# Performance work log

Hardware: AMD Instinct MI355X
Metric: run time of the kernel (lower is better)

The kernel has to match this reference:

```python
import jax, jax.numpy as jnp
import numpy as np

VOXEL_SIZE = np.array([0.05, 0.05, 0.1], dtype=np.float32)
PCR = np.array([0.0, -40.0, -3.0, 70.4, 40.0, 1.0], dtype=np.float32)
MAX_POINTS = 32
MAX_VOXELS = 120000
N_POINTS = 2_000_000
NFEAT = 4

GRID = np.round((PCR[3:] - PCR[:3]) / VOXEL_SIZE).astype(np.int64)  # [gx, gy, gz] = [1408, 1600, 40]
GX, GY, GZ = int(GRID[0]), int(GRID[1]), int(GRID[2])
G_TOTAL = GX * GY * GZ  # sentinel linear id for invalid points


def setup_inputs() -> dict:
    key = jax.random.key(0)
    k1, k2 = jax.random.split(key)
    # xyz uniform inside the point-cloud range, reflectivity ~ U[0,1)
    xyz = jax.random.uniform(k1, (N_POINTS, 3), minval=jnp.asarray(PCR[:3]), maxval=jnp.asarray(PCR[3:]))
    feat = jax.random.uniform(k2, (N_POINTS, NFEAT - 3))
    points = jnp.concatenate([xyz, feat], axis=1).astype(jnp.float32)
    return {"points": points}


def reference(points):
    """Deterministic hard voxelization (mmcv hard_voxelize_forward).

    Returns padded fixed-shape outputs plus voxel_num (jit-compatible):
      voxels [MAX_VOXELS, MAX_POINTS, C], coors [MAX_VOXELS, 3] (z,y,x),
      num_points_per_voxel [MAX_VOXELS], voxel_num scalar.
    Rows >= voxel_num are zero padding (torch version slices them off).
    """
    N, C = points.shape
    vs = jnp.asarray(VOXEL_SIZE)
    lo = jnp.asarray(PCR[:3])

    # Voxel coordinate of each point (x, y, z order)
    c = jnp.floor((points[:, :3] - lo) / vs).astype(jnp.int32)  # [N,3]
    valid = jnp.all((c >= 0) & (c < jnp.array([GX, GY, GZ], jnp.int32)), axis=1)

    # Linear voxel id; invalid points -> sentinel G_TOTAL (sorts last)
    lin = (c[:, 2].astype(jnp.int64) * (GY * GX)
           + c[:, 1].astype(jnp.int64) * GX
           + c[:, 0].astype(jnp.int64))
    lin = jnp.where(valid, lin, G_TOTAL)

    # Stable sort by voxel id: within a voxel, points keep original order
    order = jnp.argsort(lin, stable=True)          # [N] original indices
    slin = lin[order]
    pos = jnp.arange(N)
    is_new = jnp.concatenate([jnp.array([True]), slin[1:] != slin[:-1]])  # group starts
    start_pos = jax.lax.cummax(jnp.where(is_new, pos, 0))  # start position of each point's group
    rank_in_group = pos - start_pos                         # arrival order within voxel
    valid_s = slin < G_TOTAL

    # Voxel slots are assigned in order of first point appearance (deterministic CUDA kernel).
    # At each group start, the group's first original point index is order[pos].
    group_key = jnp.where(is_new & valid_s, order, N)       # non-starts/invalid rank last
    slot_at_pos = jnp.argsort(jnp.argsort(group_key))       # rank among groups by first appearance
    slot = slot_at_pos[start_pos]                            # [N] voxel slot per point

    voxel_num = jnp.minimum(jnp.sum((is_new & valid_s).astype(jnp.int32)), MAX_VOXELS)

    keep = valid_s & (rank_in_group < MAX_POINTS) & (slot < MAX_VOXELS)
    slot_w = jnp.where(keep, slot, MAX_VOXELS)   # dropped points -> extra pad row
    rank_w = jnp.where(keep, rank_in_group, 0)

    voxels = jnp.zeros((MAX_VOXELS + 1, MAX_POINTS, C), points.dtype)
    voxels = voxels.at[slot_w, rank_w].set(points[order])[:MAX_VOXELS]

    czyx = c[order][:, ::-1]  # store coords in (z, y, x) order like mmcv
    coor_keep = is_new & valid_s & (slot < MAX_VOXELS)
    cslot = jnp.where(coor_keep, slot, MAX_VOXELS)
    coors = jnp.zeros((MAX_VOXELS + 1, 3), jnp.int32).at[cslot].set(czyx)[:MAX_VOXELS]

    num_points_per_voxel = (jnp.zeros((MAX_VOXELS + 1,), jnp.int32)
                            .at[slot_w].add(keep.astype(jnp.int32))[:MAX_VOXELS])

    return voxels, coors, num_points_per_voxel, voxel_num
```

## Files before the change

kernel.cpp:

```cpp
#include <hip/hip_runtime.h>


#define GX 1408
#define GY 1600
#define GZ 40
#define MAXV 120000
#define MAXP 32

#define CSHIFT 19
#define NCB 172
#define CCAP 14336
#define FSHIFT 15
#define NFB 2750
#define BCAP 1024
#define TSIZE 2048
#define TMASK (TSIZE - 1)
#define PB 4

#define ABLK 512
#define APT 8
#define EMIT_SPB 8

typedef unsigned long long u64;
typedef unsigned int u32;
#define EMPTY64 0xFFFFFFFFFFFFFFFFull

__device__ __forceinline__ u32 hashw(u32 lin) {
  return (lin * 2654435761u) >> 21 & TMASK;
}

__global__ __launch_bounds__(ABLK) void k_binA(const float4* __restrict__ pts,
                                               u64* __restrict__ cpairs,
                                               u32* __restrict__ ccnt, int n) {
  __shared__ u32 hist[NCB];
  __shared__ u32 cursor[NCB];
  int tid = threadIdx.x;
  if (tid < NCB) hist[tid] = 0;
  __syncthreads();

  int base0 = blockIdx.x * (ABLK * APT) + tid;
  int lin[APT];
#pragma unroll
  for (int j = 0; j < APT; ++j) {
    int i = base0 + j * ABLK;
    lin[j] = -1;
    if (i < n) {
      float4 p = pts[i];
      int cx = (int)floorf((p.x - 0.0f)   / 0.05f);
      int cy = (int)floorf((p.y - -40.0f) / 0.05f);
      int cz = (int)floorf((p.z - -3.0f)  / 0.1f);
      if ((cx >= 0) && (cx < GX) && (cy >= 0) && (cy < GY) && (cz >= 0) && (cz < GZ)) {
        lin[j] = cz * (GX * GY) + cy * GX + cx;
        atomicAdd(&hist[(u32)lin[j] >> CSHIFT], 1u);
      }
    }
  }
  __syncthreads();
  if (tid < NCB) {
    u32 c = hist[tid];
    cursor[tid] = c ? atomicAdd(&ccnt[tid], c) : 0u;
  }
  __syncthreads();
#pragma unroll
  for (int j = 0; j < APT; ++j) {
    if (lin[j] >= 0) {
      int i = base0 + j * ABLK;
      u32 c = (u32)lin[j] >> CSHIFT;
      u32 pos = atomicAdd(&cursor[c], 1u);
      if (pos < CCAP) cpairs[(size_t)c * CCAP + pos] = ((u64)(u32)lin[j] << 32) | (u32)i;
    }
  }
}

__global__ __launch_bounds__(1024) void k_binB(const u64* __restrict__ cpairs,
                                               const u32* __restrict__ ccnt,
                                               u64* __restrict__ fpairs,
                                               u32* __restrict__ fcnt) {
  __shared__ u32 fh[16], fcur[16];
  int tid = threadIdx.x;
  int c = blockIdx.x;
  if (tid < 16) { fh[tid] = 0; fcur[tid] = 0; }
  __syncthreads();

  u32 cnt = ccnt[c];
  if (cnt > CCAP) cnt = CCAP;
  size_t base = (size_t)c * CCAP;

  for (u32 j = tid; j < cnt; j += 1024) {
    u32 lin = (u32)(cpairs[base + j] >> 32);
    atomicAdd(&fh[(lin >> FSHIFT) & 15], 1u);
  }
  __syncthreads();
  if (tid < 16 && c * 16 + tid < NFB) fcnt[c * 16 + tid] = fh[tid];
  __syncthreads();
  for (u32 j = tid; j < cnt; j += 1024) {
    u64 pr = cpairs[base + j];
    u32 f = ((u32)(pr >> 32) >> FSHIFT) & 15;
    u32 pos = atomicAdd(&fcur[f], 1u);
    if (pos < BCAP) fpairs[(size_t)(c * 16 + f) * BCAP + pos] = pr;
  }
}

__global__ __launch_bounds__(256) void k_build(const u64* __restrict__ fpairs,
                                               const u32* __restrict__ fcnt,
                                               u32* __restrict__ Lvals,
                                               unsigned char* __restrict__ isleader) {
  __shared__ u64 tab[TSIZE];
  int tid = threadIdx.x;
  int b = blockIdx.x;
  for (int s = tid; s < TSIZE; s += 256) tab[s] = EMPTY64;
  __syncthreads();

  u32 cnt = fcnt[b];
  if (cnt > BCAP) cnt = BCAP;
  size_t base = (size_t)b * BCAP;

  u64 pr[PB]; u32 hh[PB]; u64 old[PB];
#pragma unroll
  for (int k = 0; k < PB; ++k) {
    u32 idx = (u32)tid + (u32)k * 256u;
    pr[k] = (idx < cnt) ? fpairs[base + idx] : EMPTY64;
  }
#pragma unroll
  for (int k = 0; k < PB; ++k) {
    if (pr[k] != EMPTY64) {
      hh[k] = hashw((u32)(pr[k] >> 32));
      old[k] = atomicCAS(&tab[hh[k]], EMPTY64, pr[k]);
    }
  }
#pragma unroll
  for (int k = 0; k < PB; ++k) {
    if (pr[k] != EMPTY64) {
      u32 lin = (u32)(pr[k] >> 32), i = (u32)pr[k];
      u32 s = hh[k];
      u64 o = old[k];
      while (o != EMPTY64) {
        if ((u32)(o >> 32) == lin) {
          while ((u32)o > i) {
            u64 want = (o & 0xFFFFFFFF00000000ull) | (u64)i;
            u64 prev = atomicCAS(&tab[s], o, want);
            if (prev == o) break;
            o = prev;
          }
          break;
        }
        s = (s + 1) & TMASK;
        o = atomicCAS(&tab[s], EMPTY64, pr[k]);
      }
    }
  }
  __syncthreads();

#pragma unroll
  for (int k = 0; k < PB; ++k) {
    if (pr[k] != EMPTY64) {
      u32 idx = (u32)tid + (u32)k * 256u;
      u32 lin = (u32)(pr[k] >> 32), i = (u32)pr[k];
      u32 s = hashw(lin);
      u64 e = tab[s];
      while ((u32)(e >> 32) != lin) { s = (s + 1) & TMASK; e = tab[s]; }
      u32 L = (u32)e;
      Lvals[base + idx] = L;
      if (L == i) isleader[i] = 1;
    }
  }
}

__global__ __launch_bounds__(256) void k_rankA(const unsigned char* __restrict__ isl,
                                               u32* __restrict__ flag,
                                               u32* __restrict__ bsum, int nwords) {
  __shared__ u32 red[256];
  int t = threadIdx.x;
  int w = blockIdx.x * 256 + t;
  u32 bits = 0;
  if (w < nwords) {
    const uint4* p = (const uint4*)(isl + (size_t)w * 32);
    uint4 a = p[0], b4 = p[1];
    u32 wd[8] = {a.x, a.y, a.z, a.w, b4.x, b4.y, b4.z, b4.w};
#pragma unroll
    for (int k = 0; k < 8; ++k) {
      u32 v = wd[k];
      bits |= (((v >> 0) & 1u) | ((v >> 8) & 1u) << 1 |
               ((v >> 16) & 1u) << 2 | ((v >> 24) & 1u) << 3) << (4 * k);
    }
    flag[w] = bits;
  }
  red[t] = __popc(bits);
  __syncthreads();
  for (int off = 128; off > 0; off >>= 1) {
    if (t < off) red[t] += red[t + off];
    __syncthreads();
  }
  if (t == 0) bsum[blockIdx.x] = red[0];
}

__global__ __launch_bounds__(256) void k_rankC(const u32* __restrict__ flag,
                                               const u32* __restrict__ bsum,
                                               u32* __restrict__ wordpfx,
                                               float* __restrict__ voxnum_out,
                                               int* __restrict__ lmax,
                                               int nwords, int nbk) {
  __shared__ u32 sb_[256];
  __shared__ u32 sm[256];
  int t = threadIdx.x;
  sb_[t] = (t < nbk) ? bsum[t] : 0;
  __syncthreads();
  for (int off = 1; off < 256; off <<= 1) {
    u32 x = sb_[t];
    u32 add = (t >= off) ? sb_[t - off] : 0;
    __syncthreads();
    sb_[t] = x + add;
    __syncthreads();
  }
  u32 blockoff = (blockIdx.x > 0) ? sb_[blockIdx.x - 1] : 0u;
  u32 total = sb_[nbk - 1];

  int w = blockIdx.x * 256 + t;
  u32 bits = (w < nwords) ? flag[w] : 0u;
  u32 c = __popc(bits);
  sm[t] = c;
  __syncthreads();
  for (int off = 1; off < 256; off <<= 1) {
    u32 x = sm[t];
    u32 add = (t >= off) ? sm[t - off] : 0;
    __syncthreads();
    sm[t] = x + add;
    __syncthreads();
  }
  u32 p = blockoff + sm[t] - c;
  if (w < nwords) {
    wordpfx[w] = p;
    if (p < MAXV && p + c >= MAXV) {
      int kth = MAXV - 1 - (int)p;
      u32 ww = bits;
      while (kth > 0) { ww &= ww - 1; --kth; }
      *lmax = (w << 5) | (__ffs(ww) - 1);
    }
  }
  if (blockIdx.x == 0 && t == 0) {
    *voxnum_out = (float)(total < MAXV ? total : (u32)MAXV);
    if (total < MAXV) *lmax = 0x7FFFFFFF;
  }
}

__global__ __launch_bounds__(256) void k_keep(const u64* __restrict__ fpairs,
                                              const u32* __restrict__ fcnt,
                                              const u32* __restrict__ Lvals,
                                              const u32* __restrict__ flag,
                                              const u32* __restrict__ wordpfx,
                                              const int* __restrict__ lmaxp,
                                              int* __restrict__ bcnt,
                                              int* __restrict__ bucket,
                                              float* __restrict__ out_coors) {
  int tid = threadIdx.x;
  int b = blockIdx.x;
  u32 Lmax = (u32)*lmaxp;
  u32 cnt = fcnt[b];
  if (cnt > BCAP) cnt = BCAP;
  size_t base = (size_t)b * BCAP;

  for (u32 j = tid; j < cnt; j += 256) {
    u32 L = Lvals[base + j];
    if (L > Lmax) continue;
    u64 pr = fpairs[base + j];
    u32 lin = (u32)(pr >> 32), i = (u32)pr;
    u32 w = L >> 5;
    u32 r = wordpfx[w] + __popc(flag[w] & ((1u << (L & 31)) - 1u));
    int pos = atomicAdd(&bcnt[r], 1);
    if (pos < MAXP) bucket[r * MAXP + pos] = (int)i;
    if (i == L) {
      int li = (int)lin;
      int x = li % GX;
      int t2 = li / GX;
      int y = t2 % GY;
      int z = t2 / GY;
      out_coors[r * 3 + 0] = (float)z;
      out_coors[r * 3 + 1] = (float)y;
      out_coors[r * 3 + 2] = (float)x;
    }
  }
}

__global__ __launch_bounds__(256) void k_emit(const float4* __restrict__ pts,
                                              const int* __restrict__ bcnt,
                                              const int* __restrict__ bucket,
                                              float4* __restrict__ out_voxels,
                                              float* __restrict__ out_npts) {
  __shared__ int sb[EMIT_SPB][MAXP];
  int grp = threadIdx.x >> 5;
  int r = threadIdx.x & 31;
  int s = blockIdx.x * EMIT_SPB + grp;

  int nfull = bcnt[s];
  int m = nfull < MAXP ? nfull : MAXP;
  if (r < m) sb[grp][r] = bucket[s * MAXP + r];
  __syncthreads();

  float4 row = make_float4(0.f, 0.f, 0.f, 0.f);
  if (r < m) {
    int mine = -1;
    for (int jj = 0; jj < m; ++jj) {
      int ej = sb[grp][jj];
      int rk = 0;
      for (int kk2 = 0; kk2 < m; ++kk2) rk += (sb[grp][kk2] < ej) ? 1 : 0;
      if (rk == r) mine = ej;
    }
    row = pts[mine];
  }
  out_voxels[(size_t)s * MAXP + r] = row;
  if (r == 0) out_npts[s] = (float)m;
}

extern "C" void kernel_launch(void* const* d_in, const int* in_sizes, int n_in,
                              void* d_out, int out_size, void* d_ws, size_t ws_size,
                              hipStream_t stream) {
  const float4* pts = (const float4*)d_in[0];
  int n = in_sizes[0] / 4;
  float* out = (float*)d_out;
  int nwords = (n + 31) / 32;
  int nbk = (nwords + 255) / 256;

  char* ws = (char*)d_ws;
  size_t off = 0;
  auto alloc = [&](size_t bytes) { void* p = ws + off; off += (bytes + 255) & ~(size_t)255; return p; };
  u64* cpairs   = (u64*)alloc((size_t)NCB * CCAP * 8);
  u64* fpairs   = (u64*)alloc((size_t)NFB * BCAP * 8);
  u32* Lvals    = (u32*)alloc((size_t)NFB * BCAP * 4);
  unsigned char* isleader = (unsigned char*)alloc((size_t)n);
  u32* flag     = (u32*)alloc(262144);
  u32* wordpfx  = (u32*)alloc(262144);
  u32* bsum     = (u32*)alloc(1024);
  int* lmax     = (int*)alloc(256);
  u32* ccnt     = (u32*)alloc((size_t)NCB * 4 + (size_t)NFB * 4 + (size_t)MAXV * 4);
  u32* fcnt     = ccnt + NCB;
  int* bcnt     = (int*)(fcnt + NFB);
  int* bucket   = (int*)alloc((size_t)MAXV * MAXP * 4);

  float* out_voxels = out;
  float* out_coors  = out + (size_t)MAXV * MAXP * 4;
  float* out_npts   = out_coors + (size_t)MAXV * 3;

  hipMemsetAsync(ccnt, 0, ((size_t)NCB + NFB + MAXV) * 4, stream);
  hipMemsetAsync(isleader, 0, (size_t)n, stream);
  hipMemsetAsync(out_coors, 0, ((size_t)MAXV * 3 + MAXV + 1) * sizeof(float), stream);

  int nb_binA = (n + ABLK * APT - 1) / (ABLK * APT);

  k_binA<<<nb_binA, ABLK, 0, stream>>>(pts, cpairs, ccnt, n);
  k_binB<<<NCB, 1024, 0, stream>>>(cpairs, ccnt, fpairs, fcnt);
  k_build<<<NFB, 256, 0, stream>>>(fpairs, fcnt, Lvals, isleader);
  k_rankA<<<nbk, 256, 0, stream>>>(isleader, flag, bsum, nwords);
  k_rankC<<<nbk, 256, 0, stream>>>(flag, bsum, wordpfx, out_npts + MAXV, lmax, nwords, nbk);
  k_keep<<<NFB, 256, 0, stream>>>(fpairs, fcnt, Lvals, flag, wordpfx, lmax,
                                  bcnt, bucket, out_coors);
  k_emit<<<MAXV / EMIT_SPB, 256, 0, stream>>>(
      pts, bcnt, bucket, (float4*)out_voxels, out_npts);
}
```

Before: 177.2 us.

## Replace two-pass coarse/fine binning with single-pass binning into 8 sub-groups

The binning kernel now histograms points straight into the 2750 fine buckets in shared memory and scatters them into one of 8 per-block-group sub-buckets, so the intermediate coarse-bucket pass (k_binB) and its extra write and read of all pairs go away. Splitting each fine bucket across 8 groups reduces contention on the global cursor atomics. The build and keep kernels now loop over the 8 sub-groups per bucket instead of using a fixed 4-per-thread register batch. The costs are a larger shared-memory histogram, more global cursor atomics per block, lost batching in the hash build, and a per-group capacity of 192 that could overflow on skewed inputs.

```diff
diff --git a/kernel.cpp b/kernel.cpp
--- a/kernel.cpp
+++ b/kernel.cpp
@@ -7,15 +7,13 @@
 #define MAXV 120000
 #define MAXP 32
 
-#define CSHIFT 19
-#define NCB 172
-#define CCAP 14336
 #define FSHIFT 15
 #define NFB 2750
-#define BCAP 1024
+#define NGR 8
+#define GCAP 192
+#define GSTRIDE 2816
 #define TSIZE 2048
 #define TMASK (TSIZE - 1)
-#define PB 4
 
 #define ABLK 512
 #define APT 8
@@ -30,12 +28,13 @@
 }
 
 __global__ __launch_bounds__(ABLK) void k_binA(const float4* __restrict__ pts,
-                                               u64* __restrict__ cpairs,
-                                               u32* __restrict__ ccnt, int n) {
-  __shared__ u32 hist[NCB];
-  __shared__ u32 cursor[NCB];
+                                               u64* __restrict__ fpairs,
+                                               u32* __restrict__ gcur, int n) {
+  __shared__ u32 hist[NFB];
+  __shared__ u32 cur[NFB];
   int tid = threadIdx.x;
-  if (tid < NCB) hist[tid] = 0;
+  u32 g = (u32)blockIdx.x & (NGR - 1);
+  for (int b = tid; b < NFB; b += ABLK) hist[b] = 0;
   __syncthreads();
 
   int base0 = blockIdx.x * (ABLK * APT) + tid;
@@ -51,58 +50,30 @@
       int cz = (int)floorf((p.z - -3.0f)  / 0.1f);
       if ((cx >= 0) && (cx < GX) && (cy >= 0) && (cy < GY) && (cz >= 0) && (cz < GZ)) {
         lin[j] = cz * (GX * GY) + cy * GX + cx;
-        atomicAdd(&hist[(u32)lin[j] >> CSHIFT], 1u);
+        atomicAdd(&hist[(u32)lin[j] >> FSHIFT], 1u);
       }
     }
   }
   __syncthreads();
-  if (tid < NCB) {
-    u32 c = hist[tid];
-    cursor[tid] = c ? atomicAdd(&ccnt[tid], c) : 0u;
+  for (int b = tid; b < NFB; b += ABLK) {
+    u32 c = hist[b];
+    cur[b] = c ? atomicAdd(&gcur[g * GSTRIDE + b], c) : 0u;
   }
   __syncthreads();
 #pragma unroll
   for (int j = 0; j < APT; ++j) {
     if (lin[j] >= 0) {
       int i = base0 + j * ABLK;
-      u32 c = (u32)lin[j] >> CSHIFT;
-      u32 pos = atomicAdd(&cursor[c], 1u);
-      if (pos < CCAP) cpairs[(size_t)c * CCAP + pos] = ((u64)(u32)lin[j] << 32) | (u32)i;
-    }
-  }
-}
-
-__global__ __launch_bounds__(1024) void k_binB(const u64* __restrict__ cpairs,
-                                               const u32* __restrict__ ccnt,
-                                               u64* __restrict__ fpairs,
-                                               u32* __restrict__ fcnt) {
-  __shared__ u32 fh[16], fcur[16];
-  int tid = threadIdx.x;
-  int c = blockIdx.x;
-  if (tid < 16) { fh[tid] = 0; fcur[tid] = 0; }
-  __syncthreads();
-
-  u32 cnt = ccnt[c];
-  if (cnt > CCAP) cnt = CCAP;
-  size_t base = (size_t)c * CCAP;
-
-  for (u32 j = tid; j < cnt; j += 1024) {
-    u32 lin = (u32)(cpairs[base + j] >> 32);
-    atomicAdd(&fh[(lin >> FSHIFT) & 15], 1u);
-  }
-  __syncthreads();
-  if (tid < 16 && c * 16 + tid < NFB) fcnt[c * 16 + tid] = fh[tid];
-  __syncthreads();
-  for (u32 j = tid; j < cnt; j += 1024) {
-    u64 pr = cpairs[base + j];
-    u32 f = ((u32)(pr >> 32) >> FSHIFT) & 15;
-    u32 pos = atomicAdd(&fcur[f], 1u);
-    if (pos < BCAP) fpairs[(size_t)(c * 16 + f) * BCAP + pos] = pr;
+      u32 b = (u32)lin[j] >> FSHIFT;
+      u32 pos = atomicAdd(&cur[b], 1u);
+      if (pos < GCAP)
+        fpairs[((size_t)g * NFB + b) * GCAP + pos] = ((u64)(u32)lin[j] << 32) | (u32)i;
+    }
   }
 }
 
 __global__ __launch_bounds__(256) void k_build(const u64* __restrict__ fpairs,
-                                               const u32* __restrict__ fcnt,
+                                               const u32* __restrict__ gcur,
                                                u32* __restrict__ Lvals,
                                                unsigned char* __restrict__ isleader) {
   __shared__ u64 tab[TSIZE];
@@ -111,29 +82,15 @@
   for (int s = tid; s < TSIZE; s += 256) tab[s] = EMPTY64;
   __syncthreads();
 
-  u32 cnt = fcnt[b];
-  if (cnt > BCAP) cnt = BCAP;
-  size_t base = (size_t)b * BCAP;
-
-  u64 pr[PB]; u32 hh[PB]; u64 old[PB];
-#pragma unroll
-  for (int k = 0; k < PB; ++k) {
-    u32 idx = (u32)tid + (u32)k * 256u;
-    pr[k] = (idx < cnt) ? fpairs[base + idx] : EMPTY64;
-  }
-#pragma unroll
-  for (int k = 0; k < PB; ++k) {
-    if (pr[k] != EMPTY64) {
-      hh[k] = hashw((u32)(pr[k] >> 32));
-      old[k] = atomicCAS(&tab[hh[k]], EMPTY64, pr[k]);
-    }
-  }
-#pragma unroll
-  for (int k = 0; k < PB; ++k) {
-    if (pr[k] != EMPTY64) {
-      u32 lin = (u32)(pr[k] >> 32), i = (u32)pr[k];
-      u32 s = hh[k];
-      u64 o = old[k];
+  for (int g = 0; g < NGR; ++g) {
+    u32 cg = gcur[g * GSTRIDE + b];
+    if (cg > GCAP) cg = GCAP;
+    size_t base = ((size_t)g * NFB + b) * GCAP;
+    for (u32 j = tid; j < cg; j += 256) {
+      u64 pr = fpairs[base + j];
+      u32 lin = (u32)(pr >> 32), i = (u32)pr;
+      u32 s = hashw(lin);
+      u64 o = atomicCAS(&tab[s], EMPTY64, pr);
       while (o != EMPTY64) {
         if ((u32)(o >> 32) == lin) {
           while ((u32)o > i) {
@@ -145,22 +102,24 @@
           break;
         }
         s = (s + 1) & TMASK;
-        o = atomicCAS(&tab[s], EMPTY64, pr[k]);
+        o = atomicCAS(&tab[s], EMPTY64, pr);
       }
     }
   }
   __syncthreads();
 
-#pragma unroll
-  for (int k = 0; k < PB; ++k) {
-    if (pr[k] != EMPTY64) {
-      u32 idx = (u32)tid + (u32)k * 256u;
-      u32 lin = (u32)(pr[k] >> 32), i = (u32)pr[k];
+  for (int g = 0; g < NGR; ++g) {
+    u32 cg = gcur[g * GSTRIDE + b];
+    if (cg > GCAP) cg = GCAP;
+    size_t base = ((size_t)g * NFB + b) * GCAP;
+    for (u32 j = tid; j < cg; j += 256) {
+      u64 pr = fpairs[base + j];
+      u32 lin = (u32)(pr >> 32), i = (u32)pr;
       u32 s = hashw(lin);
       u64 e = tab[s];
       while ((u32)(e >> 32) != lin) { s = (s + 1) & TMASK; e = tab[s]; }
       u32 L = (u32)e;
-      Lvals[base + idx] = L;
+      Lvals[base + j] = L;
       if (L == i) isleader[i] = 1;
     }
   }
@@ -244,7 +203,7 @@
 }
 
 __global__ __launch_bounds__(256) void k_keep(const u64* __restrict__ fpairs,
-                                              const u32* __restrict__ fcnt,
+                                              const u32* __restrict__ gcur,
                                               const u32* __restrict__ Lvals,
                                               const u32* __restrict__ flag,
                                               const u32* __restrict__ wordpfx,
@@ -255,28 +214,30 @@
   int tid = threadIdx.x;
   int b = blockIdx.x;
   u32 Lmax = (u32)*lmaxp;
-  u32 cnt = fcnt[b];
-  if (cnt > BCAP) cnt = BCAP;
-  size_t base = (size_t)b * BCAP;
-
-  for (u32 j = tid; j < cnt; j += 256) {
-    u32 L = Lvals[base + j];
-    if (L > Lmax) continue;
-    u64 pr = fpairs[base + j];
-    u32 lin = (u32)(pr >> 32), i = (u32)pr;
-    u32 w = L >> 5;
-    u32 r = wordpfx[w] + __popc(flag[w] & ((1u << (L & 31)) - 1u));
-    int pos = atomicAdd(&bcnt[r], 1);
-    if (pos < MAXP) bucket[r * MAXP + pos] = (int)i;
-    if (i == L) {
-      int li = (int)lin;
-      int x = li % GX;
-      int t2 = li / GX;
-      int y = t2 % GY;
-      int z = t2 / GY;
-      out_coors[r * 3 + 0] = (float)z;
-      out_coors[r * 3 + 1] = (float)y;
-      out_coors[r * 3 + 2] = (float)x;
+
+  for (int g = 0; g < NGR; ++g) {
+    u32 cg = gcur[g * GSTRIDE + b];
+    if (cg > GCAP) cg = GCAP;
+    size_t base = ((size_t)g * NFB + b) * GCAP;
+    for (u32 j = tid; j < cg; j += 256) {
+      u32 L = Lvals[base + j];
+      if (L > Lmax) continue;
+      u64 pr = fpairs[base + j];
+      u32 lin = (u32)(pr >> 32), i = (u32)pr;
+      u32 w = L >> 5;
+      u32 r = wordpfx[w] + __popc(flag[w] & ((1u << (L & 31)) - 1u));
+      int pos = atomicAdd(&bcnt[r], 1);
+      if (pos < MAXP) bucket[r * MAXP + pos] = (int)i;
+      if (i == L) {
+        int li = (int)lin;
+        int x = li % GX;
+        int t2 = li / GX;
+        int y = t2 % GY;
+        int z = t2 / GY;
+        out_coors[r * 3 + 0] = (float)z;
+        out_coors[r * 3 + 1] = (float)y;
+        out_coors[r * 3 + 2] = (float)x;
+      }
     }
   }
 }
@@ -323,35 +284,32 @@
   char* ws = (char*)d_ws;
   size_t off = 0;
   auto alloc = [&](size_t bytes) { void* p = ws + off; off += (bytes + 255) & ~(size_t)255; return p; };
-  u64* cpairs   = (u64*)alloc((size_t)NCB * CCAP * 8);
-  u64* fpairs   = (u64*)alloc((size_t)NFB * BCAP * 8);
-  u32* Lvals    = (u32*)alloc((size_t)NFB * BCAP * 4);
+  u64* fpairs   = (u64*)alloc((size_t)NGR * NFB * GCAP * 8);
+  u32* Lvals    = (u32*)alloc((size_t)NGR * NFB * GCAP * 4);
   unsigned char* isleader = (unsigned char*)alloc((size_t)n);
   u32* flag     = (u32*)alloc(262144);
   u32* wordpfx  = (u32*)alloc(262144);
   u32* bsum     = (u32*)alloc(1024);
   int* lmax     = (int*)alloc(256);
-  u32* ccnt     = (u32*)alloc((size_t)NCB * 4 + (size_t)NFB * 4 + (size_t)MAXV * 4);
-  u32* fcnt     = ccnt + NCB;
-  int* bcnt     = (int*)(fcnt + NFB);
+  u32* gcur     = (u32*)alloc((size_t)NGR * GSTRIDE * 4 + (size_t)MAXV * 4);
+  int* bcnt     = (int*)(gcur + (size_t)NGR * GSTRIDE);
   int* bucket   = (int*)alloc((size_t)MAXV * MAXP * 4);
 
   float* out_voxels = out;
   float* out_coors  = out + (size_t)MAXV * MAXP * 4;
   float* out_npts   = out_coors + (size_t)MAXV * 3;
 
-  hipMemsetAsync(ccnt, 0, ((size_t)NCB + NFB + MAXV) * 4, stream);
+  hipMemsetAsync(gcur, 0, ((size_t)NGR * GSTRIDE + MAXV) * 4, stream);
   hipMemsetAsync(isleader, 0, (size_t)n, stream);
   hipMemsetAsync(out_coors, 0, ((size_t)MAXV * 3 + MAXV + 1) * sizeof(float), stream);
 
   int nb_binA = (n + ABLK * APT - 1) / (ABLK * APT);
 
-  k_binA<<<nb_binA, ABLK, 0, stream>>>(pts, cpairs, ccnt, n);
-  k_binB<<<NCB, 1024, 0, stream>>>(cpairs, ccnt, fpairs, fcnt);
-  k_build<<<NFB, 256, 0, stream>>>(fpairs, fcnt, Lvals, isleader);
+  k_binA<<<nb_binA, ABLK, 0, stream>>>(pts, fpairs, gcur, n);
+  k_build<<<NFB, 256, 0, stream>>>(fpairs, gcur, Lvals, isleader);
   k_rankA<<<nbk, 256, 0, stream>>>(isleader, flag, bsum, nwords);
   k_rankC<<<nbk, 256, 0, stream>>>(flag, bsum, wordpfx, out_npts + MAXV, lmax, nwords, nbk);
-  k_keep<<<NFB, 256, 0, stream>>>(fpairs, fcnt, Lvals, flag, wordpfx, lmax,
+  k_keep<<<NFB, 256, 0, stream>>>(fpairs, gcur, Lvals, flag, wordpfx, lmax,
                                   bcnt, bucket, out_coors);
   k_emit<<<MAXV / EMIT_SPB, 256, 0, stream>>>(
       pts, bcnt, bucket, (float4*)out_voxels, out_npts);
```

After: 170.7 us. 1.04x faster.
